# Performance work log

Measured on AMD Instinct MI355X. Metric: run time of the kernel, lower is better.

The kernel has to match this reference:

```python
import jax, jax.numpy as jnp
import numpy as np

T, B = 256, 512
IN, NG = 512, 5
H, LAT = 2048, 1024


def gru_cell(x, h, w_ih, w_hh, b_ih, b_hh):
    # torch.nn.GRUCell math
    gi = x @ w_ih.T + b_ih            # [B, 3H]
    gh = h @ w_hh.T + b_hh            # [B, 3H]
    ir, iz, inn = jnp.split(gi, 3, axis=-1)
    hr, hz, hn = jnp.split(gh, 3, axis=-1)
    r = jax.nn.sigmoid(ir + hr)
    z = jax.nn.sigmoid(iz + hz)
    n = jnp.tanh(inn + r * hn)
    return (1.0 - z) * n + z * h


def setup_inputs() -> dict:
    key = jax.random.key(0)
    ks = jax.random.split(key, 20)
    s = 0.02
    d = {
        "x": jax.random.normal(ks[0], (T, B, IN + NG), jnp.float32),
        "latent_genre_vec": jax.random.uniform(ks[1], (B, NG), jnp.float32),
        "eps": jax.random.normal(ks[2], (B, LAT - NG), jnp.float32),
        "enc_w_ih": s * jax.random.normal(ks[3], (3 * H, IN + NG), jnp.float32),
        "enc_w_hh": s * jax.random.normal(ks[4], (3 * H, H), jnp.float32),
        "enc_b_ih": jnp.zeros((3 * H,), jnp.float32),
        "enc_b_hh": jnp.zeros((3 * H,), jnp.float32),
        "dec_w_ih": s * jax.random.normal(ks[5], (3 * H, IN), jnp.float32),
        "dec_w_hh": s * jax.random.normal(ks[6], (3 * H, H), jnp.float32),
        "dec_b_ih": jnp.zeros((3 * H,), jnp.float32),
        "dec_b_hh": jnp.zeros((3 * H,), jnp.float32),
        "fc_mu_w": s * jax.random.normal(ks[7], (LAT - NG, H), jnp.float32),
        "fc_mu_b": jnp.zeros((LAT - NG,), jnp.float32),
        "fc_logvar_w": s * jax.random.normal(ks[8], (LAT - NG, H), jnp.float32),
        "fc_logvar_b": jnp.zeros((LAT - NG,), jnp.float32),
        "fc_output_w": s * jax.random.normal(ks[9], (H, LAT), jnp.float32),
        "fc_output_b": jnp.zeros((H,), jnp.float32),
        "fc_decoder_w": s * jax.random.normal(ks[10], (IN, H), jnp.float32),
        "fc_decoder_b": jnp.zeros((IN,), jnp.float32),
    }
    return d


def reference(x, latent_genre_vec, eps,
              enc_w_ih, enc_w_hh, enc_b_ih, enc_b_hh,
              dec_w_ih, dec_w_hh, dec_b_ih, dec_b_hh,
              fc_mu_w, fc_mu_b, fc_logvar_w, fc_logvar_b,
              fc_output_w, fc_output_b, fc_decoder_w, fc_decoder_b):
    Bsz = x.shape[1]
    h0 = jnp.zeros((Bsz, enc_w_hh.shape[1]), x.dtype)

    # encoder: sequential GRU over time
    def enc_step(h, xt):
        return gru_cell(xt, h, enc_w_ih, enc_w_hh, enc_b_ih, enc_b_hh), None
    h_enc, _ = jax.lax.scan(enc_step, h0, x)

    mu = h_enc @ fc_mu_w.T + fc_mu_b
    logvar = h_enc @ fc_logvar_w.T + fc_logvar_b
    z = mu + jnp.exp(0.5 * logvar) * eps
    z = jnp.concatenate((z, latent_genre_vec), axis=1)
    h_dec0 = z @ fc_output_w.T + fc_output_b

    note0 = jnp.zeros((Bsz, fc_decoder_w.shape[0]), x.dtype)

    def dec_step(carry, _):
        h, note = carry
        h = gru_cell(note, h, dec_w_ih, dec_w_hh, dec_b_ih, dec_b_hh)
        note = h @ fc_decoder_w.T + fc_decoder_b
        return (h, note), note

    _, output = jax.lax.scan(dec_step, (h_dec0, note0), None, length=x.shape[0])
    return output, mu, logvar
```

## Files before the change

kernel.cpp:

```cpp
#include <hip/hip_runtime.h>
#include <hip/hip_bf16.h>

typedef __bf16 bf16_t;
typedef bf16_t bfx8 __attribute__((ext_vector_type(8)));
typedef float  fx4  __attribute__((ext_vector_type(4)));

#define TT     256
#define BB     512
#define INDIM  512
#define NGENRE 5
#define HD     2048
#define LATD   1024
#define LATM   1019
#define XK     517
#define XKP    576

__device__ __forceinline__ bf16_t f2b(float f) {
  unsigned u = __builtin_bit_cast(unsigned, f);
  u += 0x7fffu + ((u >> 16) & 1u);
  unsigned short s = (unsigned short)(u >> 16);
  return __builtin_bit_cast(bf16_t, s);
}
__device__ __forceinline__ float sigmoidf_(float x) { return 1.0f / (1.0f + __expf(-x)); }

__device__ __forceinline__ void gload16(const bf16_t* g, bf16_t* l) {
  __builtin_amdgcn_global_load_lds((const __attribute__((address_space(1))) void*)g,
                                   (__attribute__((address_space(3))) void*)l,
                                   16, 0, 0);
}
__device__ __forceinline__ void wait_vm0()  { asm volatile("s_waitcnt vmcnt(0)" ::: "memory"); }
__device__ __forceinline__ void wait_vm4()  { asm volatile("s_waitcnt vmcnt(4)" ::: "memory"); }
__device__ __forceinline__ void wait_vm5()  { asm volatile("s_waitcnt vmcnt(5)" ::: "memory"); }
__device__ __forceinline__ void wait_vm6()  { asm volatile("s_waitcnt vmcnt(6)" ::: "memory"); }
__device__ __forceinline__ void wait_vm10() { asm volatile("s_waitcnt vmcnt(10)" ::: "memory"); }
__device__ __forceinline__ void wait_vm12() { asm volatile("s_waitcnt vmcnt(12)" ::: "memory"); }
__device__ __forceinline__ void wait_lgkm0() { asm volatile("s_waitcnt lgkmcnt(0)" ::: "memory"); }

__global__ void wcast_pad(const float* __restrict__ src, bf16_t* __restrict__ dst,
                          int rows_src, int rows_pad, int K, int ldp) {
  for (int r = blockIdx.x; r < rows_pad; r += gridDim.x)
    for (int c = threadIdx.x; c < ldp; c += 256)
      dst[(size_t)r * ldp + c] = (r < rows_src && c < K) ? f2b(src[(size_t)r * K + c]) : f2b(0.0f);
}

__global__ __launch_bounds__(256, 2)
void gru6(const bf16_t* __restrict__ A1, int lda1, int k1s,
          const bf16_t* __restrict__ Wih, int ldwih,
          const bf16_t* __restrict__ Hb,
          const bf16_t* __restrict__ Whh,
          const float* __restrict__ Hin,
          const float* __restrict__ bih, const float* __restrict__ bhh,
          float* __restrict__ Hout, bf16_t* __restrict__ HoutB)
{
  __shared__ bf16_t aT[3][128 * 64];
  __shared__ bf16_t bT[3][48 * 64];
  const int tid = threadIdx.x, wv = tid >> 6, lane = tid & 63;
  const int bid = blockIdx.x;
  const int xcd = bid & 7, loc = bid >> 3;
  const int j0 = (xcd * 16 + (loc >> 2)) * 16;
  const int m0 = (loc & 3) * 128;
  const int lr = lane & 15, lk = lane >> 4;
  const int rl = lane >> 3;
  const int cl = (lane & 7) * 8;

  fx4 acc[2][4];
#pragma unroll
  for (int m = 0; m < 2; ++m)
#pragma unroll
    for (int g = 0; g < 4; ++g) acc[m][g] = fx4{0.f, 0.f, 0.f, 0.f};

  const bf16_t* A1b = A1 ? A1 : Hb;

  int aOff0[4], aOff1[4], aSlot[4];
#pragma unroll
  for (int i = 0; i < 4; ++i) {
    const int t = wv * 4 + i;
    const int r = t * 8 + rl;
    const int c = cl ^ ((r & 7) * 8);
    aOff0[i] = (m0 + r) * lda1 + c;
    aOff1[i] = (m0 + r) * HD + c;
    aSlot[i] = t * 512;
  }
  const int nB  = (wv < 2) ? 2 : 1;
  const int bt0 = (wv < 2) ? wv * 2 : (2 + wv);
  int bOff0[2], bOff1[2], bSlot[2];
#pragma unroll
  for (int i = 0; i < 2; ++i) {
    const int t = bt0 + (i < nB ? i : 0);
    const int r = t * 8 + rl;
    const int g = r >> 4, jj = r & 15;
    const int c = cl ^ ((r & 7) * 8);
    bOff0[i] = (g * HD + j0 + jj) * ldwih + c;
    bOff1[i] = (g * HD + j0 + jj) * HD + c;
    bSlot[i] = t * 512;
  }

  int aRow[2], bRow[3], ko[2];
#pragma unroll
  for (int m = 0; m < 2; ++m) aRow[m] = (wv * 32 + m * 16 + lr) * 64;
#pragma unroll
  for (int g = 0; g < 3; ++g) bRow[g] = (g * 16 + lr) * 64;
#pragma unroll
  for (int h = 0; h < 2; ++h) ko[h] = (h * 32 + lk * 8) ^ ((lr & 7) * 8);

  auto stage = [&](int buf, int s) {
    const bool p = (s >= k1s);
    const int kb = (p ? (s - k1s) : s) * 64;
    bf16_t* aD = &aT[buf][0];
    bf16_t* bD = &bT[buf][0];
    if (p) {
#pragma unroll
      for (int i = 0; i < 4; ++i) gload16(Hb + aOff1[i] + kb, aD + aSlot[i]);
      gload16(Whh + bOff1[0] + kb, bD + bSlot[0]);
      if (wv < 2) gload16(Whh + bOff1[1] + kb, bD + bSlot[1]);
    } else {
#pragma unroll
      for (int i = 0; i < 4; ++i) gload16(A1b + aOff0[i] + kb, aD + aSlot[i]);
      gload16(Wih + bOff0[0] + kb, bD + bSlot[0]);
      if (wv < 2) gload16(Wih + bOff0[1] + kb, bD + bSlot[1]);
    }
  };

  const int nk = k1s + HD / 64;
  stage(0, 0); stage(1, 1); stage(2, 2);
  int buf = 0;
  for (int s = 0; s < nk; ++s) {
    const int rem = nk - 1 - s;
    if (rem >= 2)      { if (wv < 2) wait_vm12(); else wait_vm10(); }
    else if (rem == 1) { if (wv < 2) wait_vm6();  else wait_vm5();  }
    else               wait_vm0();
    __builtin_amdgcn_s_barrier();
    const bf16_t* aB = &aT[buf][0];
    const bf16_t* bB = &bT[buf][0];
    bfx8 af[2][2], bfr[3][2];
#pragma unroll
    for (int m = 0; m < 2; ++m)
#pragma unroll
      for (int h = 0; h < 2; ++h)
        af[m][h] = *reinterpret_cast<const bfx8*>(&aB[aRow[m] + ko[h]]);
#pragma unroll
    for (int g = 0; g < 3; ++g)
#pragma unroll
      for (int h = 0; h < 2; ++h)
        bfr[g][h] = *reinterpret_cast<const bfx8*>(&bB[bRow[g] + ko[h]]);
    wait_lgkm0();
    __builtin_amdgcn_sched_barrier(0);
    __builtin_amdgcn_s_barrier();
    if (s + 3 < nk) stage(buf, s + 3);
    const bool p = (s >= k1s);
    __builtin_amdgcn_s_setprio(1);
#pragma unroll
    for (int h = 0; h < 2; ++h)
#pragma unroll
      for (int g = 0; g < 3; ++g) {
        const int slot = (g == 2) ? (p ? 3 : 2) : g;
#pragma unroll
        for (int m = 0; m < 2; ++m)
          acc[m][slot] = __builtin_amdgcn_mfma_f32_16x16x32_bf16(af[m][h], bfr[g][h], acc[m][slot], 0, 0, 0);
      }
    __builtin_amdgcn_s_setprio(0);
    buf = (buf == 2) ? 0 : buf + 1;
  }

  const int col = j0 + lr;
  const float br  = bih[col] + bhh[col];
  const float bz  = bih[HD + col] + bhh[HD + col];
  const float bin = bih[2 * HD + col];
  const float bhn = bhh[2 * HD + col];
#pragma unroll
  for (int m = 0; m < 2; ++m) {
    const int rbase = m0 + wv * 32 + m * 16 + lk * 4;
#pragma unroll
    for (int q = 0; q < 4; ++q) {
      const int row = rbase + q;
      const float r = sigmoidf_(acc[m][0][q] + br);
      const float z = sigmoidf_(acc[m][1][q] + bz);
      const float n = tanhf(acc[m][2][q] + bin + r * (acc[m][3][q] + bhn));
      const float hv = (1.0f - z) * n + z * Hin[(size_t)row * HD + col];
      Hout[(size_t)row * HD + col]  = hv;
      HoutB[(size_t)row * HD + col] = f2b(hv);
    }
  }
}

__global__ __launch_bounds__(256, 2)
void gemm_nt3(const bf16_t* __restrict__ A, int lda, int K,
              const bf16_t* __restrict__ W, int ldw,
              const float* __restrict__ bias,
              float* __restrict__ O, int ldo, int N,
              bf16_t* __restrict__ OB, int ldob)
{
  __shared__ bf16_t aT[2][64 * 64];
  __shared__ bf16_t bT[2][64 * 64];
  const int tid = threadIdx.x, wave = tid >> 6, lane = tid & 63;
  const int m0 = blockIdx.y * 64, n0 = blockIdx.x * 64;
  const int wm = wave & 1, wn = wave >> 1;
  const int lr = lane & 15, lk = lane >> 4;
  const int rl = lane >> 3, cl = (lane & 7) * 8;

  fx4 acc[2][2];
#pragma unroll
  for (int a = 0; a < 2; ++a)
#pragma unroll
    for (int b = 0; b < 2; ++b) acc[a][b] = fx4{0.f, 0.f, 0.f, 0.f};

  const bf16_t* pA[2]; const bf16_t* pB[2]; int slot[2];
#pragma unroll
  for (int i = 0; i < 2; ++i) {
    const int t = wave * 2 + i;
    const int r = t * 8 + rl;
    const int c = cl ^ ((r & 7) * 8);
    pA[i] = A + (size_t)(m0 + r) * lda + c;
    pB[i] = W + (size_t)(n0 + r) * ldw + c;
    slot[i] = t * 512;
  }
  int aRow[2], bRow[2], ko[2];
#pragma unroll
  for (int f = 0; f < 2; ++f) {
    aRow[f] = (wm * 32 + f * 16 + lr) * 64;
    bRow[f] = (wn * 32 + f * 16 + lr) * 64;
  }
#pragma unroll
  for (int h = 0; h < 2; ++h) ko[h] = (h * 32 + lk * 8) ^ ((lr & 7) * 8);

  auto stage = [&](int buf, int kb) {
#pragma unroll
    for (int i = 0; i < 2; ++i) {
      gload16(pA[i] + kb, &aT[buf][slot[i]]);
      gload16(pB[i] + kb, &bT[buf][slot[i]]);
    }
  };

  const int nk = K >> 6;
  stage(0, 0);
  stage(1, 64);
  for (int s = 0; s < nk; ++s) {
    if (s == nk - 1) wait_vm0(); else wait_vm4();
    __builtin_amdgcn_s_barrier();
    const bf16_t* aB = &aT[s & 1][0];
    const bf16_t* bB = &bT[s & 1][0];
    bfx8 af[2][2], bfr[2][2];
#pragma unroll
    for (int f = 0; f < 2; ++f)
#pragma unroll
      for (int h = 0; h < 2; ++h) {
        af[f][h]  = *reinterpret_cast<const bfx8*>(&aB[aRow[f] + ko[h]]);
        bfr[f][h] = *reinterpret_cast<const bfx8*>(&bB[bRow[f] + ko[h]]);
      }
    wait_lgkm0();
    __builtin_amdgcn_sched_barrier(0);
    __builtin_amdgcn_s_barrier();
    if (s + 2 < nk) stage(s & 1, (s + 2) << 6);
    __builtin_amdgcn_s_setprio(1);
#pragma unroll
    for (int h = 0; h < 2; ++h)
#pragma unroll
      for (int fm = 0; fm < 2; ++fm)
#pragma unroll
        for (int fj = 0; fj < 2; ++fj)
          acc[fm][fj] = __builtin_amdgcn_mfma_f32_16x16x32_bf16(af[fm][h], bfr[fj][h], acc[fm][fj], 0, 0, 0);
    __builtin_amdgcn_s_setprio(0);
  }

#pragma unroll
  for (int fm = 0; fm < 2; ++fm)
#pragma unroll
    for (int fj = 0; fj < 2; ++fj) {
      const int col = n0 + wn * 32 + fj * 16 + lr;
      if (col < N) {
        const float bb = bias[col];
#pragma unroll
        for (int q = 0; q < 4; ++q) {
          const int row = m0 + wm * 32 + fm * 16 + lk * 4 + q;
          const float v = acc[fm][fj][q] + bb;
          O[(size_t)row * ldo + col] = v;
          if (OB) OB[(size_t)row * ldob + col] = f2b(v);
        }
      }
    }
}

__global__ void build_zb(const float* __restrict__ mu, const float* __restrict__ lv,
                         const float* __restrict__ eps, const float* __restrict__ genre,
                         bf16_t* __restrict__ zb) {
  int i = blockIdx.x * 256 + threadIdx.x;
  int b = i >> 10, c = i & 1023;
  float v;
  if (c < LATM) {
    size_t k = (size_t)b * LATM + c;
    v = mu[k] + expf(0.5f * lv[k]) * eps[k];
  } else {
    v = genre[b * NGENRE + (c - LATM)];
  }
  zb[i] = f2b(v);
}

__global__ __launch_bounds__(256, 1)
void gru_stepF(const float* __restrict__ A1, int lda1, int K1,
               const float* __restrict__ Wih,
               const float* __restrict__ Hin,
               const float* __restrict__ Whh,
               const float* __restrict__ bih, const float* __restrict__ bhh,
               float* __restrict__ Hout)
{
  __shared__ bf16_t a_lds[128][32];
  __shared__ bf16_t b_lds[96][32];
  const int tid = threadIdx.x, wave = tid >> 6, lane = tid & 63;
  const int m0 = (blockIdx.x >> 6) * 128, j0 = (blockIdx.x & 63) * 32;
  const int lr = lane & 15, lk = lane >> 4;
  fx4 acc[2][2][4];
#pragma unroll
  for (int a = 0; a < 2; ++a)
#pragma unroll
    for (int b = 0; b < 2; ++b)
#pragma unroll
      for (int g = 0; g < 4; ++g) acc[a][b][g] = fx4{0.f, 0.f, 0.f, 0.f};

  for (int ph = 0; ph < 2; ++ph) {
    const float* Ag = ph ? Hin : A1;
    const int lda = ph ? HD : lda1, kLen = ph ? HD : K1;
    const float* W = ph ? Whh : Wih;
    const int nslot = ph ? 3 : 2;
    const int nkk = (kLen + 31) >> 5;
    for (int s = 0; s < nkk; ++s) {
      const int kb = s << 5;
#pragma unroll
      for (int it = 0; it < 16; ++it) {
        int i = tid + it * 256;
        int r = i >> 5, kk = i & 31, gk = kb + kk;
        float v = 0.0f;
        if (Ag && gk < kLen) v = Ag[(size_t)(m0 + r) * lda + gk];
        a_lds[r][kk] = f2b(v);
      }
#pragma unroll
      for (int it = 0; it < 12; ++it) {
        int i = tid + it * 256;
        int r = i >> 5, kk = i & 31, g = r >> 5, jj = r & 31, gk = kb + kk;
        b_lds[r][kk] = (gk < kLen) ? f2b(W[(size_t)(g * HD + j0 + jj) * kLen + gk]) : f2b(0.0f);
      }
      __syncthreads();
      bfx8 af[2];
#pragma unroll
      for (int fm = 0; fm < 2; ++fm)
        af[fm] = *reinterpret_cast<const bfx8*>(&a_lds[wave * 32 + fm * 16 + lr][lk * 8]);
#pragma unroll
      for (int g = 0; g < 3; ++g) {
        const int slot = (g == 2) ? nslot : g;
#pragma unroll
        for (int fj = 0; fj < 2; ++fj) {
          bfx8 bfr = *reinterpret_cast<const bfx8*>(&b_lds[g * 32 + fj * 16 + lr][lk * 8]);
#pragma unroll
          for (int fm = 0; fm < 2; ++fm)
            acc[fm][fj][slot] = __builtin_amdgcn_mfma_f32_16x16x32_bf16(af[fm], bfr, acc[fm][fj][slot], 0, 0, 0);
        }
      }
      __syncthreads();
    }
  }
#pragma unroll
  for (int fj = 0; fj < 2; ++fj) {
    const int col = j0 + fj * 16 + lr;
    const float br = bih[col] + bhh[col];
    const float bz = bih[HD + col] + bhh[HD + col];
    const float bin = bih[2 * HD + col];
    const float bhn = bhh[2 * HD + col];
#pragma unroll
    for (int fm = 0; fm < 2; ++fm) {
      const int rbase = m0 + wave * 32 + fm * 16 + lk * 4;
#pragma unroll
      for (int q = 0; q < 4; ++q) {
        const int row = rbase + q;
        const float r = sigmoidf_(acc[fm][fj][0][q] + br);
        const float z = sigmoidf_(acc[fm][fj][1][q] + bz);
        const float n = tanhf(acc[fm][fj][2][q] + bin + r * (acc[fm][fj][3][q] + bhn));
        Hout[(size_t)row * HD + col] = (1.0f - z) * n + z * Hin[(size_t)row * HD + col];
      }
    }
  }
}

__global__ __launch_bounds__(256, 1)
void gemm_ntF(const float* __restrict__ A, int lda, int K,
              const float* __restrict__ W,
              const float* __restrict__ bias,
              float* __restrict__ O, int ldo, int N)
{
  __shared__ bf16_t a_lds[64][32];
  __shared__ bf16_t b_lds[64][32];
  const int tid = threadIdx.x, wave = tid >> 6, lane = tid & 63;
  const int m0 = blockIdx.y * 64, n0 = blockIdx.x * 64;
  const int wm = (wave & 1) * 32, wn = (wave >> 1) * 32;
  const int lr = lane & 15, lk = lane >> 4;
  fx4 acc[2][2];
#pragma unroll
  for (int a = 0; a < 2; ++a)
#pragma unroll
    for (int b = 0; b < 2; ++b) acc[a][b] = fx4{0.f, 0.f, 0.f, 0.f};
  for (int kb = 0; kb < K; kb += 32) {
#pragma unroll
    for (int it = 0; it < 8; ++it) {
      int i = tid + it * 256;
      int r = i >> 5, kk = i & 31;
      a_lds[r][kk] = f2b(A[(size_t)(m0 + r) * lda + kb + kk]);
    }
#pragma unroll
    for (int it = 0; it < 8; ++it) {
      int i = tid + it * 256;
      int r = i >> 5, kk = i & 31;
      int n = n0 + r;
      b_lds[r][kk] = (n < N) ? f2b(W[(size_t)n * K + kb + kk]) : f2b(0.0f);
    }
    __syncthreads();
    bfx8 af[2], bfr[2];
#pragma unroll
    for (int f = 0; f < 2; ++f) {
      af[f] = *reinterpret_cast<const bfx8*>(&a_lds[wm + f * 16 + lr][lk * 8]);
      bfr[f] = *reinterpret_cast<const bfx8*>(&b_lds[wn + f * 16 + lr][lk * 8]);
    }
#pragma unroll
    for (int fm = 0; fm < 2; ++fm)
#pragma unroll
      for (int fj = 0; fj < 2; ++fj)
        acc[fm][fj] = __builtin_amdgcn_mfma_f32_16x16x32_bf16(af[fm], bfr[fj], acc[fm][fj], 0, 0, 0);
    __syncthreads();
  }
#pragma unroll
  for (int fm = 0; fm < 2; ++fm)
#pragma unroll
    for (int fj = 0; fj < 2; ++fj) {
      const int col = n0 + wn + fj * 16 + lr;
      if (col < N) {
        const float bb = bias[col];
#pragma unroll
        for (int q = 0; q < 4; ++q) {
          const int row = m0 + wm + fm * 16 + lk * 4 + q;
          O[(size_t)row * ldo + col] = acc[fm][fj][q] + bb;
        }
      }
    }
}

__global__ void build_zf(const float* __restrict__ mu, const float* __restrict__ lv,
                         const float* __restrict__ eps, const float* __restrict__ genre,
                         float* __restrict__ z) {
  int i = blockIdx.x * 256 + threadIdx.x;
  int b = i >> 10, c = i & 1023;
  z[i] = (c < LATM) ? mu[(size_t)b * LATM + c] + expf(0.5f * lv[(size_t)b * LATM + c]) * eps[(size_t)b * LATM + c]
                    : genre[b * NGENRE + (c - LATM)];
}

extern "C" void kernel_launch(void* const* d_in, const int* in_sizes, int n_in,
                              void* d_out, int out_size, void* d_ws, size_t ws_size,
                              hipStream_t stream) {
  const float* x      = (const float*)d_in[0];
  const float* genre  = (const float*)d_in[1];
  const float* eps    = (const float*)d_in[2];
  const float* eWih   = (const float*)d_in[3];
  const float* eWhh   = (const float*)d_in[4];
  const float* eBih   = (const float*)d_in[5];
  const float* eBhh   = (const float*)d_in[6];
  const float* dWih   = (const float*)d_in[7];
  const float* dWhh   = (const float*)d_in[8];
  const float* dBih   = (const float*)d_in[9];
  const float* dBhh   = (const float*)d_in[10];
  const float* fcMuW  = (const float*)d_in[11];
  const float* fcMuB  = (const float*)d_in[12];
  const float* fcLvW  = (const float*)d_in[13];
  const float* fcLvB  = (const float*)d_in[14];
  const float* fcOutW = (const float*)d_in[15];
  const float* fcOutB = (const float*)d_in[16];
  const float* fcDecW = (const float*)d_in[17];
  const float* fcDecB = (const float*)d_in[18];

  float* out = (float*)d_out;
  float* muO = out + (size_t)TT * BB * INDIM;
  float* lvO = muO + (size_t)BB * LATM;

  const size_t nEih = (size_t)3 * HD * XKP;
  const size_t nEhh = (size_t)3 * HD * HD;
  const size_t nDih = (size_t)3 * HD * INDIM;
  const size_t nDhh = (size_t)3 * HD * HD;
  const size_t nMu  = (size_t)1024 * HD;
  const size_t nOut = (size_t)HD * LATD;
  const size_t nDec = (size_t)INDIM * HD;
  const size_t oEih = 0;
  const size_t oEhh = oEih + nEih;
  const size_t oDih = oEhh + nEhh;
  const size_t oDhh = oDih + nDih;
  const size_t oMu  = oDhh + nDhh;
  const size_t oLv  = oMu + nMu;
  const size_t oOut = oLv + nMu;
  const size_t oDec = oOut + nOut;
  const size_t wTot = oDec + nDec;

  const size_t bytesW  = wTot * 2;
  const size_t bytesHF = (size_t)BB * HD * 4;
  const size_t bytesHB = (size_t)BB * HD * 2;
  const size_t bytesZB = (size_t)BB * LATD * 2;
  const size_t bytesNB = (size_t)BB * INDIM * 2;
  const size_t bytesX1 = (size_t)BB * XKP * 2;
  const size_t bytesXB = (size_t)TT * BB * XKP * 2;
  const size_t needB = bytesW + 2 * bytesHF + 2 * bytesHB + bytesZB + bytesNB + bytesX1 + 1024;
  const size_t needA = needB + bytesXB;

  if (ws_size >= needB) {
    const bool haveXB = (ws_size >= needA);
    char* p = (char*)d_ws;
    bf16_t* wb = (bf16_t*)p;            p += bytesW;
    float* h0  = (float*)p;             p += bytesHF;
    float* h1  = (float*)p;             p += bytesHF;
    bf16_t* hb0 = (bf16_t*)p;           p += bytesHB;
    bf16_t* hb1 = (bf16_t*)p;           p += bytesHB;
    bf16_t* zb  = (bf16_t*)p;           p += bytesZB;
    bf16_t* nb  = (bf16_t*)p;           p += bytesNB;
    bf16_t* x1  = (bf16_t*)p;           p += bytesX1;
    bf16_t* xb  = haveXB ? (bf16_t*)p : nullptr;

    auto cast = [&](const float* s, bf16_t* d, int rs, int rp, int K, int ldp) {
      int g = rp > 8192 ? 8192 : rp;
      wcast_pad<<<g, 256, 0, stream>>>(s, d, rs, rp, K, ldp);
    };
    cast(eWih,   wb + oEih, 3 * HD, 3 * HD, XK,    XKP);
    cast(eWhh,   wb + oEhh, 3 * HD, 3 * HD, HD,    HD);
    cast(dWih,   wb + oDih, 3 * HD, 3 * HD, INDIM, INDIM);
    cast(dWhh,   wb + oDhh, 3 * HD, 3 * HD, HD,    HD);
    cast(fcMuW,  wb + oMu,  LATM,   1024,   HD,    HD);
    cast(fcLvW,  wb + oLv,  LATM,   1024,   HD,    HD);
    cast(fcOutW, wb + oOut, HD,     HD,     LATD,  LATD);
    cast(fcDecW, wb + oDec, INDIM,  INDIM,  HD,    HD);
    if (haveXB) cast(x, xb, TT * BB, TT * BB, XK, XKP);

    hipMemsetAsync(h0, 0, bytesHF, stream);
    hipMemsetAsync(hb0, 0, bytesHB, stream);

    float*  hF[2] = {h0, h1};
    bf16_t* hB[2] = {hb0, hb1};

    for (int t = 0; t < TT; ++t) {
      const int ci = t & 1, co = ci ^ 1;
      const bf16_t* xt;
      if (haveXB) {
        xt = xb + (size_t)t * BB * XKP;
      } else {
        wcast_pad<<<512, 256, 0, stream>>>(x + (size_t)t * BB * XK, x1, BB, BB, XK, XKP);
        xt = x1;
      }
      gru6<<<512, 256, 0, stream>>>(xt, XKP, XKP / 64,
                                    wb + oEih, XKP, hB[ci], wb + oEhh,
                                    hF[ci], eBih, eBhh, hF[co], hB[co]);
    }
    gemm_nt3<<<dim3(16, 8), 256, 0, stream>>>(hB[0], HD, HD, wb + oMu, HD, fcMuB,
                                              muO, LATM, LATM, nullptr, 0);
    gemm_nt3<<<dim3(16, 8), 256, 0, stream>>>(hB[0], HD, HD, wb + oLv, HD, fcLvB,
                                              lvO, LATM, LATM, nullptr, 0);
    build_zb<<<(BB * LATD) / 256, 256, 0, stream>>>(muO, lvO, eps, genre, zb);
    gemm_nt3<<<dim3(32, 8), 256, 0, stream>>>(zb, LATD, LATD, wb + oOut, LATD, fcOutB,
                                              hF[0], HD, HD, hB[0], HD);
    for (int t = 0; t < TT; ++t) {
      const int ci = t & 1, co = ci ^ 1;
      gru6<<<512, 256, 0, stream>>>(t ? nb : (const bf16_t*)nullptr, INDIM,
                                    t ? INDIM / 64 : 0,
                                    wb + oDih, INDIM, hB[ci], wb + oDhh,
                                    hF[ci], dBih, dBhh, hF[co], hB[co]);
      gemm_nt3<<<dim3(8, 8), 256, 0, stream>>>(hB[co], HD, HD, wb + oDec, HD, fcDecB,
                                               out + (size_t)t * BB * INDIM, INDIM, INDIM,
                                               nb, INDIM);
    }
  } else {
    float* h0 = (float*)d_ws;
    float* h1 = h0 + (size_t)BB * HD;
    float* zb = h1 + (size_t)BB * HD;
    hipMemsetAsync(h0, 0, (size_t)BB * HD * sizeof(float), stream);
    float* hF[2] = {h0, h1};
    for (int t = 0; t < TT; ++t) {
      const int ci = t & 1, co = ci ^ 1;
      gru_stepF<<<256, 256, 0, stream>>>(x + (size_t)t * BB * XK, XK, XK, eWih,
                                         hF[ci], eWhh, eBih, eBhh, hF[co]);
    }
    gemm_ntF<<<dim3(16, 8), 256, 0, stream>>>(hF[0], HD, HD, fcMuW, fcMuB, muO, LATM, LATM);
    gemm_ntF<<<dim3(16, 8), 256, 0, stream>>>(hF[0], HD, HD, fcLvW, fcLvB, lvO, LATM, LATM);
    build_zf<<<(BB * LATD) / 256, 256, 0, stream>>>(muO, lvO, eps, genre, zb);
    gemm_ntF<<<dim3(32, 8), 256, 0, stream>>>(zb, LATD, LATD, fcOutW, fcOutB, hF[0], HD, HD);
    for (int t = 0; t < TT; ++t) {
      const int ci = t & 1, co = ci ^ 1;
      gru_stepF<<<256, 256, 0, stream>>>(t ? out + (size_t)(t - 1) * BB * INDIM : nullptr,
                                         INDIM, INDIM, dWih, hF[ci], dWhh, dBih, dBhh, hF[co]);
      gemm_ntF<<<dim3(8, 8), 256, 0, stream>>>(hF[co], HD, HD, fcDecW, fcDecB,
                                               out + (size_t)t * BB * INDIM, INDIM, INDIM);
    }
  }
  (void)in_sizes; (void)n_in; (void)out_size;
}
```

Before: 21.26 ms.

## Fold decoder output projection into GRU weights and batch output GEMM per chunk

Precomputes W_ih·W_dec and W_ih·b_dec so each decoder step needs only the hidden state as input. The folded input weights are merged into the r/z gates of W_hh, giving a single K=2048 GEMM over four gate blocks. The per-step note GEMM is removed and hidden states are kept in a 64-step history, so the fc_decoder projection runs as one large GEMM per chunk. This costs extra setup work and workspace, the gate GEMM gains an extra N block, and the folded bf16 weights may change numerics.

```diff
diff --git a/kernel.cpp b/kernel.cpp
--- a/kernel.cpp
+++ b/kernel.cpp
@@ -14,6 +14,7 @@
 #define LATM   1019
 #define XK     517
 #define XKP    576
+#define CHUNK  64
 
 __device__ __forceinline__ bf16_t f2b(float f) {
   unsigned u = __builtin_bit_cast(unsigned, f);
@@ -41,6 +42,165 @@
   for (int r = blockIdx.x; r < rows_pad; r += gridDim.x)
     for (int c = threadIdx.x; c < ldp; c += 256)
       dst[(size_t)r * ldp + c] = (r < rows_src && c < K) ? f2b(src[(size_t)r * K + c]) : f2b(0.0f);
+}
+
+__global__ void wtransp(const float* __restrict__ src, bf16_t* __restrict__ dst) {
+  int i = blockIdx.x * 256 + threadIdx.x;
+  int r = i >> 9, c = i & 511;
+  dst[i] = f2b(src[(size_t)c * 2048 + r]);
+}
+__global__ void bcomp(const float* __restrict__ wih, const float* __restrict__ bdec,
+                      float* __restrict__ bc) {
+  int r = blockIdx.x * 256 + threadIdx.x;
+  if (r >= 3 * HD) return;
+  float s = 0.f;
+  for (int k = 0; k < 512; ++k) s += wih[(size_t)r * 512 + k] * bdec[k];
+  bc[r] = s;
+}
+__global__ void biasbuild(const float* __restrict__ bc, const float* __restrict__ bih,
+                          const float* __restrict__ bhh,
+                          float4* __restrict__ bD, float4* __restrict__ bD0) {
+  int c = blockIdx.x * 256 + threadIdx.x;
+  if (c >= HD) return;
+  float r0 = bih[c] + bhh[c];
+  float z0 = bih[HD + c] + bhh[HD + c];
+  float i0 = bih[2 * HD + c];
+  float h0 = bhh[2 * HD + c];
+  bD0[c] = float4{r0, z0, i0, h0};
+  bD[c]  = float4{r0 + bc[c], z0 + bc[HD + c], i0 + bc[2 * HD + c], h0};
+}
+__global__ void wprime(const bf16_t* __restrict__ wc, const bf16_t* __restrict__ whh,
+                       bf16_t* __restrict__ wp, bf16_t* __restrict__ wp0) {
+  const size_t total = (size_t)4 * HD * HD;
+  for (size_t i = (size_t)blockIdx.x * 256 + threadIdx.x; i < total; i += (size_t)gridDim.x * 256) {
+    int row = (int)(i >> 11), k = (int)(i & 2047);
+    int g = row >> 11, j = row & 2047;
+    bf16_t v, v0;
+    if (g == 0) {
+      float a = (float)wc[(size_t)j * HD + k], b = (float)whh[(size_t)j * HD + k];
+      v = f2b(a + b); v0 = whh[(size_t)j * HD + k];
+    } else if (g == 1) {
+      size_t o = (size_t)(HD + j) * HD + k;
+      v = f2b((float)wc[o] + (float)whh[o]); v0 = whh[o];
+    } else if (g == 2) {
+      v = wc[(size_t)(2 * HD + j) * HD + k]; v0 = f2b(0.0f);
+    } else {
+      v = whh[(size_t)(2 * HD + j) * HD + k]; v0 = v;
+    }
+    wp[i] = v; wp0[i] = v0;
+  }
+}
+
+__global__ __launch_bounds__(256, 2)
+void gruC(const bf16_t* __restrict__ Hb,
+          const bf16_t* __restrict__ Wp,
+          const float4* __restrict__ bias4,
+          const float* __restrict__ Hin,
+          float* __restrict__ Hout, bf16_t* __restrict__ HoutB)
+{
+  __shared__ bf16_t aT[3][64 * 64];
+  __shared__ bf16_t bT[3][128 * 64];
+  const int tid = threadIdx.x, wv = tid >> 6, lane = tid & 63;
+  const int bid = blockIdx.x;
+  const int j0 = (bid & 63) * 32;
+  const int m0 = (bid >> 6) * 64;
+  const int lr = lane & 15, lk = lane >> 4;
+  const int rl = lane >> 3;
+  const int cl = (lane & 7) * 8;
+
+  fx4 acc[2][4];
+#pragma unroll
+  for (int fj = 0; fj < 2; ++fj)
+#pragma unroll
+    for (int g = 0; g < 4; ++g) acc[fj][g] = fx4{0.f, 0.f, 0.f, 0.f};
+
+  int aOff[2], aSlot[2];
+#pragma unroll
+  for (int i = 0; i < 2; ++i) {
+    const int t = wv * 2 + i;
+    const int r = t * 8 + rl;
+    const int c = cl ^ ((r & 7) * 8);
+    aOff[i] = (m0 + r) * HD + c;
+    aSlot[i] = t * 512;
+  }
+  int bOff[4], bSlot[4];
+#pragma unroll
+  for (int i = 0; i < 4; ++i) {
+    const int t = wv * 4 + i;
+    const int r = t * 8 + rl;
+    const int g = r >> 5, jj = r & 31;
+    const int c = cl ^ ((r & 7) * 8);
+    bOff[i] = (g * HD + j0 + jj) * HD + c;
+    bSlot[i] = t * 512;
+  }
+  int aRow, bRow[4][2], ko[2];
+  aRow = (wv * 16 + lr) * 64;
+#pragma unroll
+  for (int g = 0; g < 4; ++g)
+#pragma unroll
+    for (int fj = 0; fj < 2; ++fj) bRow[g][fj] = (g * 32 + fj * 16 + lr) * 64;
+#pragma unroll
+  for (int h = 0; h < 2; ++h) ko[h] = (h * 32 + lk * 8) ^ ((lr & 7) * 8);
+
+  auto stage = [&](int buf, int s) {
+    const int kb = s * 64;
+#pragma unroll
+    for (int i = 0; i < 2; ++i) gload16(Hb + aOff[i] + kb, &aT[buf][aSlot[i]]);
+#pragma unroll
+    for (int i = 0; i < 4; ++i) gload16(Wp + bOff[i] + kb, &bT[buf][bSlot[i]]);
+  };
+
+  const int nk = HD / 64;
+  stage(0, 0); stage(1, 1);
+  int rb = 0, sb = 2;
+  for (int s = 0; s < nk; ++s) {
+    if (s == nk - 1) wait_vm0(); else wait_vm6();
+    __builtin_amdgcn_s_barrier();
+    if (s + 2 < nk) stage(sb, s + 2);
+    const bf16_t* aB = &aT[rb][0];
+    const bf16_t* bB = &bT[rb][0];
+    bfx8 af[2]; bfx8 bfr[4][2][2];
+#pragma unroll
+    for (int h = 0; h < 2; ++h)
+      af[h] = *reinterpret_cast<const bfx8*>(&aB[aRow + ko[h]]);
+#pragma unroll
+    for (int g = 0; g < 4; ++g)
+#pragma unroll
+      for (int fj = 0; fj < 2; ++fj)
+#pragma unroll
+        for (int h = 0; h < 2; ++h)
+          bfr[g][fj][h] = *reinterpret_cast<const bfx8*>(&bB[bRow[g][fj] + ko[h]]);
+    wait_lgkm0();
+    __builtin_amdgcn_sched_barrier(0);
+    __builtin_amdgcn_s_setprio(1);
+#pragma unroll
+    for (int h = 0; h < 2; ++h)
+#pragma unroll
+      for (int g = 0; g < 4; ++g)
+#pragma unroll
+        for (int fj = 0; fj < 2; ++fj)
+          acc[fj][g] = __builtin_amdgcn_mfma_f32_16x16x32_bf16(af[h], bfr[g][fj][h], acc[fj][g], 0, 0, 0);
+    __builtin_amdgcn_s_setprio(0);
+    rb = (rb == 2) ? 0 : rb + 1;
+    sb = (sb == 2) ? 0 : sb + 1;
+  }
+
+#pragma unroll
+  for (int fj = 0; fj < 2; ++fj) {
+    const int col = j0 + fj * 16 + lr;
+    const float4 bb = bias4[col];
+    const int rbase = m0 + wv * 16 + lk * 4;
+#pragma unroll
+    for (int q = 0; q < 4; ++q) {
+      const int row = rbase + q;
+      const float r = sigmoidf_(acc[fj][0][q] + bb.x);
+      const float z = sigmoidf_(acc[fj][1][q] + bb.y);
+      const float n = tanhf(acc[fj][2][q] + bb.z + r * (acc[fj][3][q] + bb.w));
+      const float hv = (1.0f - z) * n + z * Hin[(size_t)row * HD + col];
+      Hout[(size_t)row * HD + col]  = hv;
+      HoutB[(size_t)row * HD + col] = f2b(hv);
+    }
+  }
 }
 
 __global__ __launch_bounds__(256, 2)
@@ -94,7 +254,6 @@
     bOff1[i] = (g * HD + j0 + jj) * HD + c;
     bSlot[i] = t * 512;
   }
-
   int aRow[2], bRow[3], ko[2];
 #pragma unroll
   for (int m = 0; m < 2; ++m) aRow[m] = (wv * 32 + m * 16 + lr) * 64;
@@ -502,9 +661,20 @@
   const size_t bytesXB = (size_t)TT * BB * XKP * 2;
   const size_t needB = bytesW + 2 * bytesHF + 2 * bytesHB + bytesZB + bytesNB + bytesX1 + 1024;
   const size_t needA = needB + bytesXB;
+  const size_t bytesWdT  = (size_t)HD * 512 * 2;
+  const size_t bytesWcB  = (size_t)3 * HD * HD * 2;
+  const size_t bytesWcF  = (size_t)3 * HD * HD * 4;
+  const size_t bytesWp   = (size_t)4 * HD * HD * 2;
+  const size_t bytesBc   = (size_t)3 * HD * 4;
+  const size_t bytesB4   = (size_t)HD * 16;
+  const size_t bytesZero = (size_t)HD * 4;
+  const size_t bytesHist = (size_t)CHUNK * BB * HD * 2;
+  const size_t needC = needA + bytesWdT + bytesWcB + bytesWcF + 2 * bytesWp +
+                       bytesBc + 2 * bytesB4 + bytesZero + bytesHist + 1024;
 
   if (ws_size >= needB) {
     const bool haveXB = (ws_size >= needA);
+    const bool haveCP = (ws_size >= needC);
     char* p = (char*)d_ws;
     bf16_t* wb = (bf16_t*)p;            p += bytesW;
     float* h0  = (float*)p;             p += bytesHF;
@@ -515,6 +685,22 @@
     bf16_t* nb  = (bf16_t*)p;           p += bytesNB;
     bf16_t* x1  = (bf16_t*)p;           p += bytesX1;
     bf16_t* xb  = haveXB ? (bf16_t*)p : nullptr;
+    if (haveXB) p += bytesXB;
+    bf16_t *wdT = nullptr, *wcB = nullptr, *wP = nullptr, *wP0 = nullptr, *hist = nullptr;
+    float *wcF = nullptr, *bc = nullptr, *zerosb = nullptr;
+    float4 *b4D = nullptr, *b4D0 = nullptr;
+    if (haveCP) {
+      wdT = (bf16_t*)p;  p += bytesWdT;
+      wcB = (bf16_t*)p;  p += bytesWcB;
+      wP  = (bf16_t*)p;  p += bytesWp;
+      wP0 = (bf16_t*)p;  p += bytesWp;
+      wcF = (float*)p;   p += bytesWcF;
+      bc  = (float*)p;   p += bytesBc;
+      b4D = (float4*)p;  p += bytesB4;
+      b4D0 = (float4*)p; p += bytesB4;
+      zerosb = (float*)p; p += bytesZero;
+      hist = (bf16_t*)p; p += bytesHist;
+    }
 
     auto cast = [&](const float* s, bf16_t* d, int rs, int rp, int K, int ldp) {
       int g = rp > 8192 ? 8192 : rp;
@@ -530,6 +716,16 @@
     cast(fcDecW, wb + oDec, INDIM,  INDIM,  HD,    HD);
     if (haveXB) cast(x, xb, TT * BB, TT * BB, XK, XKP);
 
+    if (haveCP) {
+      hipMemsetAsync(zerosb, 0, bytesZero, stream);
+      wtransp<<<(HD * 512) / 256, 256, 0, stream>>>(fcDecW, wdT);
+      gemm_nt3<<<dim3(HD / 64, (3 * HD) / 64), 256, 0, stream>>>(
+          wb + oDih, INDIM, INDIM, wdT, INDIM, zerosb, wcF, HD, HD, wcB, HD);
+      bcomp<<<(3 * HD) / 256, 256, 0, stream>>>(dWih, fcDecB, bc);
+      biasbuild<<<HD / 256, 256, 0, stream>>>(bc, dBih, dBhh, b4D, b4D0);
+      wprime<<<4096, 256, 0, stream>>>(wcB, wb + oDhh, wP, wP0);
+    }
+
     hipMemsetAsync(h0, 0, bytesHF, stream);
     hipMemsetAsync(hb0, 0, bytesHB, stream);
 
@@ -556,15 +752,29 @@
     build_zb<<<(BB * LATD) / 256, 256, 0, stream>>>(muO, lvO, eps, genre, zb);
     gemm_nt3<<<dim3(32, 8), 256, 0, stream>>>(zb, LATD, LATD, wb + oOut, LATD, fcOutB,
                                               hF[0], HD, HD, hB[0], HD);
-    for (int t = 0; t < TT; ++t) {
-      const int ci = t & 1, co = ci ^ 1;
-      gru6<<<512, 256, 0, stream>>>(t ? nb : (const bf16_t*)nullptr, INDIM,
-                                    t ? INDIM / 64 : 0,
-                                    wb + oDih, INDIM, hB[ci], wb + oDhh,
-                                    hF[ci], dBih, dBhh, hF[co], hB[co]);
-      gemm_nt3<<<dim3(8, 8), 256, 0, stream>>>(hB[co], HD, HD, wb + oDec, HD, fcDecB,
-                                               out + (size_t)t * BB * INDIM, INDIM, INDIM,
-                                               nb, INDIM);
+    if (haveCP) {
+      for (int t = 0; t < TT; ++t) {
+        const bf16_t* hprev = (t == 0) ? hB[0] : hist + (size_t)((t - 1) & (CHUNK - 1)) * BB * HD;
+        gruC<<<512, 256, 0, stream>>>(hprev, t ? wP : wP0, t ? b4D : b4D0,
+                                      hF[t & 1], hF[(t & 1) ^ 1],
+                                      hist + (size_t)(t & (CHUNK - 1)) * BB * HD);
+        if ((t & (CHUNK - 1)) == CHUNK - 1) {
+          gemm_nt3<<<dim3(INDIM / 64, (CHUNK * BB) / 64), 256, 0, stream>>>(
+              hist, HD, HD, wb + oDec, HD, fcDecB,
+              out + (size_t)(t - (CHUNK - 1)) * BB * INDIM, INDIM, INDIM, nullptr, 0);
+        }
+      }
+    } else {
+      for (int t = 0; t < TT; ++t) {
+        const int ci = t & 1, co = ci ^ 1;
+        gru6<<<512, 256, 0, stream>>>(t ? nb : (const bf16_t*)nullptr, INDIM,
+                                      t ? INDIM / 64 : 0,
+                                      wb + oDih, INDIM, hB[ci], wb + oDhh,
+                                      hF[ci], dBih, dBhh, hF[co], hB[co]);
+        gemm_nt3<<<dim3(8, 8), 256, 0, stream>>>(hB[co], HD, HD, wb + oDec, HD, fcDecB,
+                                                 out + (size_t)t * BB * INDIM, INDIM, INDIM,
+                                                 nb, INDIM);
+      }
     }
   } else {
     float* h0 = (float*)d_ws;
```

After: 17.12 ms. 1.24x faster.
